# Kernel tuning notes

Measured on AMD Instinct MI355X. Metric: run time of the kernel, lower is better.

Reference implementation:

```python
import jax, jax.numpy as jnp
import numpy as np
import math

N, E, D, H, C, G = 100000, 1600000, 256, 256, 4, 512
LN_EPS = 1e-5


def _pe(n, d):
    # sinusoidal positional encoding, rows = node index
    pos = jnp.arange(n, dtype=jnp.float32)[:, None]                      # [n,1]
    div = jnp.exp(jnp.arange(0, d, 2, dtype=jnp.float32) * (-math.log(10000.0) / d))  # [d/2]
    ang = pos * div                                                      # [n,d/2]
    return jnp.stack([jnp.sin(ang), jnp.cos(ang)], axis=-1).reshape(n, d)


def setup_inputs() -> dict:
    key = jax.random.key(0)
    ks = jax.random.split(key, 24)
    w = lambda k, shp: (jax.random.normal(k, shp, jnp.float32) * 0.05)
    inp = {
        "x": jax.random.normal(ks[0], (N, D), jnp.float32),
        "W_ft": w(ks[1], (D, H)), "b_ft": jnp.zeros((H,), jnp.float32),
        "ln_g": jnp.ones((H,), jnp.float32), "ln_b": jnp.zeros((H,), jnp.float32),
        "W_g0": w(ks[2], (H, H)), "b_g0": jnp.zeros((H,), jnp.float32),
        "W_g1": w(ks[3], (H, H)), "b_g1": jnp.zeros((H,), jnp.float32),
        "W_g2": w(ks[4], (H, H)), "b_g2": jnp.zeros((H,), jnp.float32),
        "W_c0": w(ks[5], (H, H)), "b_c0": jnp.zeros((H,), jnp.float32),
        "W_c1": w(ks[6], (H, H // 2)), "b_c1": jnp.zeros((H // 2,), jnp.float32),
        "W_c2": w(ks[7], (H // 2, C)), "b_c2": jnp.zeros((C,), jnp.float32),
        "edge_index": jax.random.randint(ks[8], (2, E), 0, N, dtype=jnp.int32),
        "batch": jnp.sort(jax.random.randint(ks[9], (N,), 0, G, dtype=jnp.int32)),
    }
    return inp


def reference(x, W_ft, b_ft, ln_g, ln_b, W_g0, b_g0, W_g1, b_g1, W_g2, b_g2,
              W_c0, b_c0, W_c1, b_c1, W_c2, b_c2, edge_index, batch):
    # feature transform: Linear + ReLU + Dropout(eval) + LayerNorm
    h = jax.nn.relu(x @ W_ft + b_ft)
    mu = jnp.mean(h, axis=-1, keepdims=True)
    var = jnp.mean(jnp.square(h - mu), axis=-1, keepdims=True)
    h = (h - mu) * jax.lax.rsqrt(var + LN_EPS) * ln_g + ln_b
    # temporal positional encoding (intended per-node add)
    h = h + _pe(N, H)
    # GCN layers (PyG GCNConv: self-loops + symmetric degree norm + scatter-add)
    loops = jnp.arange(N, dtype=edge_index.dtype)
    src = jnp.concatenate([edge_index[0], loops])
    dst = jnp.concatenate([edge_index[1], loops])
    deg = jax.ops.segment_sum(jnp.ones_like(dst, dtype=h.dtype), dst, num_segments=N)
    dinv = jnp.where(deg > 0, jax.lax.rsqrt(jnp.maximum(deg, 1.0)), 0.0)
    norm = (dinv[src] * dinv[dst])[:, None]                              # [E+N,1]
    for W, b in ((W_g0, b_g0), (W_g1, b_g1), (W_g2, b_g2)):
        m = (h @ W)[src] * norm                                          # gather + scale
        h = jax.nn.relu(jax.ops.segment_sum(m, dst, num_segments=N) + b)
    # global mean pool per graph
    sums = jax.ops.segment_sum(h, batch, num_segments=G)
    cnts = jax.ops.segment_sum(jnp.ones((N,), h.dtype), batch, num_segments=G)
    pooled = sums / jnp.maximum(cnts, 1.0)[:, None]                      # [G,H]
    # classifier MLP
    z = jax.nn.relu(pooled @ W_c0 + b_c0)
    z = jax.nn.relu(z @ W_c1 + b_c1)
    return z @ W_c2 + b_c2                                               # [G,C]
```

## Files before the change

kernel.cpp:

```cpp
#include <hip/hip_runtime.h>
#include <math.h>


typedef __attribute__((ext_vector_type(8))) _Float16 half8;
typedef __attribute__((ext_vector_type(4))) float floatx4;
typedef __attribute__((ext_vector_type(8))) unsigned short us8;

union HU { _Float16 h; unsigned short u; };

static __device__ __forceinline__ unsigned short f2h(float f) {
    HU x; x.h = (_Float16)f; return x.u;
}
static __device__ __forceinline__ float h2f(unsigned short s) {
    HU x; x.u = s; return (float)x.h;
}

static __device__ __forceinline__ void gl_lds16(const void* g, void* l) {
    __builtin_amdgcn_global_load_lds(
        (const __attribute__((address_space(1))) unsigned int*)(g),
        (__attribute__((address_space(3))) unsigned int*)(l), 16, 0, 0);
}

static __device__ __forceinline__ float cw_trig(float ang, bool is_cos) {
    const float i2pi = 0.15915494309189535f;
    const float k = rintf(ang * i2pi);
    float r = fmaf(k, -6.28125f, ang);
    r = fmaf(k, -1.9352436065673828e-3f, r);
    r = fmaf(k, -6.3573019e-8f, r);
    const float rv = r * i2pi;
    return is_cos ? __builtin_amdgcn_cosf(rv) : __builtin_amdgcn_sinf(rv);
}

__global__ void tg_splitB(const float* __restrict__ W0, const float* __restrict__ W1,
                          const float* __restrict__ W2, const float* __restrict__ W3,
                          unsigned short* __restrict__ B0, unsigned short* __restrict__ B1,
                          unsigned short* __restrict__ B2, unsigned short* __restrict__ B3)
{
    const float* Ws[4] = {W0, W1, W2, W3};
    unsigned short* Bs[4] = {B0, B1, B2, B3};
    const float* W = Ws[blockIdx.z];
    unsigned short* Bt = Bs[blockIdx.z];

    __shared__ float T[64][68];
    const int tk = blockIdx.x * 64, tn = blockIdx.y * 64;
    const int t = threadIdx.x;
#pragma unroll
    for (int j = 0; j < 4; ++j) {
        const int idx = t + 256 * j;
        const int k = idx >> 4, c4 = (idx & 15) * 4;
        const float4 v = *(const float4*)&W[(size_t)(tk + k) * 256 + tn + c4];
        T[k][c4] = v.x; T[k][c4 + 1] = v.y; T[k][c4 + 2] = v.z; T[k][c4 + 3] = v.w;
    }
    __syncthreads();
#pragma unroll
    for (int j = 0; j < 4; ++j) {
        const int idx = t + 256 * j;
        const int n = idx >> 4, q = (idx & 15) * 4;
        unsigned short hh[4], ll[4];
#pragma unroll
        for (int i = 0; i < 4; ++i) {
            const float f = T[q + i][n];
            hh[i] = f2h(f);
            ll[i] = f2h(f - h2f(hh[i]));
        }
        uint2 hp, lp;
        hp.x = (unsigned)hh[0] | ((unsigned)hh[1] << 16);
        hp.y = (unsigned)hh[2] | ((unsigned)hh[3] << 16);
        lp.x = (unsigned)ll[0] | ((unsigned)ll[1] << 16);
        lp.y = (unsigned)ll[2] | ((unsigned)ll[3] << 16);
        unsigned short* row = Bt + (size_t)(tn + n) * 512;
        *(uint2*)&row[tk + q]       = hp;
        *(uint2*)&row[256 + tk + q] = lp;
    }
}

__global__ __launch_bounds__(256, 2)
void tg_ft_ln(const float* __restrict__ x, const unsigned short* __restrict__ Bt,
              const float* __restrict__ bias, const float* __restrict__ lng,
              const float* __restrict__ lnb, unsigned short* __restrict__ hh, int N)
{
    __shared__ unsigned short sAh[128 * 64];
    __shared__ unsigned short sAl[128 * 64];
    __shared__ unsigned short sB[256 * 64];
    __shared__ float sStats[128][2][2];
    __shared__ float sDiv[128];

    const int t = threadIdx.x;
    const int w = t >> 6, lane = t & 63;
    const int quad = lane >> 4, l16 = lane & 15;
    const int wr = w >> 1, wc = w & 1;
    const int row0 = blockIdx.x * 128;

    if (t < 128) sDiv[t] = expf((float)(2 * t) * -0.035977892078031970f);

    floatx4 acc[4][8];
#pragma unroll
    for (int i = 0; i < 4; ++i)
#pragma unroll
        for (int j = 0; j < 8; ++j) acc[i][j] = (floatx4){0.f, 0.f, 0.f, 0.f};

    const int arow = t >> 1;
    const int ahalf = t & 1;
    const int srow = lane >> 3;
    const int kgx  = (lane & 7) ^ srow;
    const int rsw  = l16 & 7;

    for (int k4 = 0; k4 < 4; ++k4) {
        const int ka = k4 * 64;
        if (k4) __syncthreads();
#pragma unroll
        for (int i = 0; i < 8; ++i) {
            const int rr = w * 64 + i * 8;
            gl_lds16(Bt + (size_t)(rr + srow) * 512 + ka + kgx * 8, &sB[rr * 64]);
        }
        {
            const int grow = row0 + arow;
            const bool ok = grow < N;
            const float* xp = x + (size_t)grow * 256 + ka + ahalf * 32;
#pragma unroll
            for (int j = 0; j < 4; ++j) {
                const int kg = ahalf * 4 + j;
                float4 v0 = {0.f, 0.f, 0.f, 0.f}, v1 = {0.f, 0.f, 0.f, 0.f};
                if (ok) {
                    v0 = *(const float4*)(xp + j * 8);
                    v1 = *(const float4*)(xp + j * 8 + 4);
                }
                const float f[8] = {v0.x, v0.y, v0.z, v0.w, v1.x, v1.y, v1.z, v1.w};
                us8 hi, lo;
#pragma unroll
                for (int i = 0; i < 8; ++i) {
                    hi[i] = f2h(f[i]);
                    lo[i] = f2h(f[i] - h2f(hi[i]));
                }
                const int ad = arow * 64 + ((kg ^ (arow & 7)) << 3);
                *(us8*)&sAh[ad] = hi;
                *(us8*)&sAl[ad] = lo;
            }
        }
        __syncthreads();
#pragma unroll
        for (int ks = 0; ks < 2; ++ks) {
            const int kq = ks * 4 + quad;
            half8 afh[4], afl[4];
#pragma unroll
            for (int rt = 0; rt < 4; ++rt) {
                const int r = wr * 64 + rt * 16 + l16;
                const int off = r * 64 + ((kq ^ rsw) << 3);
                afh[rt] = *(const half8*)&sAh[off];
                afl[rt] = *(const half8*)&sAl[off];
            }
#pragma unroll
            for (int cb = 0; cb < 2; ++cb) {
                half8 bfr[4];
#pragma unroll
                for (int c4 = 0; c4 < 4; ++c4) {
                    const int n = wc * 128 + (cb * 4 + c4) * 16 + l16;
                    bfr[c4] = *(const half8*)&sB[n * 64 + ((kq ^ rsw) << 3)];
                }
#pragma unroll
                for (int c4 = 0; c4 < 4; ++c4)
#pragma unroll
                    for (int rt = 0; rt < 4; ++rt) {
                        acc[rt][cb * 4 + c4] = __builtin_amdgcn_mfma_f32_16x16x32_f16(
                            afh[rt], bfr[c4], acc[rt][cb * 4 + c4], 0, 0, 0);
                        acc[rt][cb * 4 + c4] = __builtin_amdgcn_mfma_f32_16x16x32_f16(
                            afl[rt], bfr[c4], acc[rt][cb * 4 + c4], 0, 0, 0);
                    }
            }
        }
        __syncthreads();
#pragma unroll
        for (int i = 0; i < 8; ++i) {
            const int rr = w * 64 + i * 8;
            gl_lds16(Bt + (size_t)(rr + srow) * 512 + 256 + ka + kgx * 8, &sB[rr * 64]);
        }
        __syncthreads();
#pragma unroll
        for (int ks = 0; ks < 2; ++ks) {
            const int kq = ks * 4 + quad;
            half8 afh[4];
#pragma unroll
            for (int rt = 0; rt < 4; ++rt) {
                const int r = wr * 64 + rt * 16 + l16;
                afh[rt] = *(const half8*)&sAh[r * 64 + ((kq ^ rsw) << 3)];
            }
#pragma unroll
            for (int cb = 0; cb < 2; ++cb) {
                half8 bfr[4];
#pragma unroll
                for (int c4 = 0; c4 < 4; ++c4) {
                    const int n = wc * 128 + (cb * 4 + c4) * 16 + l16;
                    bfr[c4] = *(const half8*)&sB[n * 64 + ((kq ^ rsw) << 3)];
                }
#pragma unroll
                for (int c4 = 0; c4 < 4; ++c4)
#pragma unroll
                    for (int rt = 0; rt < 4; ++rt)
                        acc[rt][cb * 4 + c4] = __builtin_amdgcn_mfma_f32_16x16x32_f16(
                            afh[rt], bfr[c4], acc[rt][cb * 4 + c4], 0, 0, 0);
            }
        }
    }

    float bs[8], gs[8], bv[8], dv[8];
#pragma unroll
    for (int ct = 0; ct < 8; ++ct) {
        const int gc = wc * 128 + ct * 16 + l16;
        bs[ct] = bias[gc]; gs[ct] = lng[gc]; bv[ct] = lnb[gc];
        dv[ct] = sDiv[gc >> 1];
    }

#pragma unroll
    for (int rt = 0; rt < 4; ++rt) {
#pragma unroll
        for (int i = 0; i < 4; ++i) {
            float s = 0.f, q = 0.f;
#pragma unroll
            for (int ct = 0; ct < 8; ++ct) {
                const float v = fmaxf(acc[rt][ct][i] + bs[ct], 0.f);
                s += v; q += v * v;
            }
#pragma unroll
            for (int m = 1; m < 16; m <<= 1) {
                s += __shfl_xor(s, m, 64);
                q += __shfl_xor(q, m, 64);
            }
            if (l16 == 0) {
                const int rl = wr * 64 + rt * 16 + quad * 4 + i;
                sStats[rl][wc][0] = s;
                sStats[rl][wc][1] = q;
            }
        }
    }
    __syncthreads();

    const bool is_cos = (l16 & 1);
#pragma unroll
    for (int rt = 0; rt < 4; ++rt) {
#pragma unroll
        for (int i = 0; i < 4; ++i) {
            const int rl = wr * 64 + rt * 16 + quad * 4 + i;
            const int gr = row0 + rl;
            if (gr >= N) continue;
            const float sum = sStats[rl][0][0] + sStats[rl][1][0];
            const float sq  = sStats[rl][0][1] + sStats[rl][1][1];
            const float mu  = sum * (1.f / 256.f);
            const float var = sq * (1.f / 256.f) - mu * mu;
            const float rstd = 1.f / sqrtf(var + 1e-5f);
            const float rf = (float)gr;
            unsigned short* orow = hh + (size_t)gr * 256 + wc * 128 + l16;
#pragma unroll
            for (int ct = 0; ct < 8; ++ct) {
                const float v = fmaxf(acc[rt][ct][i] + bs[ct], 0.f);
                const float nrm = (v - mu) * rstd * gs[ct] + bv[ct];
                const float pe = cw_trig(rf * dv[ct], is_cos);
                orow[ct * 16] = f2h(nrm + pe);
            }
        }
    }
}

__global__ __launch_bounds__(256, 3)
void tg_gemm(const unsigned short* __restrict__ Ph,
             const unsigned short* __restrict__ Bt,
             const float* __restrict__ rowscale,
             unsigned short* __restrict__ out)
{
    __shared__ unsigned short sA[128 * 64], sB[128 * 64];

    const int t = threadIdx.x;
    const int w = t >> 6, lane = t & 63;
    const int quad = lane >> 4, l16 = lane & 15;
    const int wr = w >> 1, wc = w & 1;

    const int nwg = gridDim.x;
    const int swq = nwg >> 3, swr = nwg & 7;
    const int xcd = blockIdx.x & 7, oidx = blockIdx.x >> 3;
    const int lg = (xcd < swr ? xcd * (swq + 1)
                              : swr * (swq + 1) + (xcd - swr) * swq) + oidx;
    const int row0 = (lg >> 1) * 128;
    const int col0 = (lg & 1) * 128;

    floatx4 acc[4][4];
#pragma unroll
    for (int i = 0; i < 4; ++i)
#pragma unroll
        for (int j = 0; j < 4; ++j) acc[i][j] = (floatx4){0.f, 0.f, 0.f, 0.f};

    const int srow = lane >> 3;
    const int kgx  = (lane & 7) ^ srow;
    const int rsw  = l16 & 7;

    for (int c = 0; c < 8; ++c) {
        const int ka = (c >> 1) << 6;
        const int kb = ((c & 1) << 8) + ka;
        const bool stA = !(c & 1);
        if (c) __syncthreads();
#pragma unroll
        for (int i = 0; i < 4; ++i) {
            const int rr = w * 32 + i * 8;
            if (stA)
                gl_lds16(Ph + (size_t)(row0 + rr + srow) * 256 + ka + kgx * 8, &sA[rr * 64]);
            gl_lds16(Bt + (size_t)(col0 + rr + srow) * 512 + kb + kgx * 8, &sB[rr * 64]);
        }
        __syncthreads();
#pragma unroll
        for (int ks = 0; ks < 2; ++ks) {
            const int kq = ks * 4 + quad;
            half8 af[4], bfr[4];
#pragma unroll
            for (int rt = 0; rt < 4; ++rt) {
                const int r = wr * 64 + rt * 16 + l16;
                af[rt] = *(const half8*)&sA[r * 64 + ((kq ^ rsw) << 3)];
            }
#pragma unroll
            for (int ct = 0; ct < 4; ++ct) {
                const int n = wc * 64 + ct * 16 + l16;
                bfr[ct] = *(const half8*)&sB[n * 64 + ((kq ^ rsw) << 3)];
            }
#pragma unroll
            for (int ct = 0; ct < 4; ++ct)
#pragma unroll
                for (int rt = 0; rt < 4; ++rt)
                    acc[rt][ct] = __builtin_amdgcn_mfma_f32_16x16x32_f16(
                        af[rt], bfr[ct], acc[rt][ct], 0, 0, 0);
        }
    }

#pragma unroll
    for (int rt = 0; rt < 4; ++rt) {
#pragma unroll
        for (int i = 0; i < 4; ++i) {
            const int gr = row0 + wr * 64 + rt * 16 + quad * 4 + i;
            const float s = rowscale[gr];
#pragma unroll
            for (int ct = 0; ct < 4; ++ct) {
                const int gc = col0 + wc * 64 + ct * 16 + l16;
                out[(size_t)gr * 256 + gc] = f2h(acc[rt][ct][i] * s);
            }
        }
    }
}

__global__ void tg_count(const int* __restrict__ dst, int* __restrict__ deg,
                         int* __restrict__ perm, int E)
{
    const int e = blockIdx.x * blockDim.x + threadIdx.x;
    if (e < E) perm[e] = atomicAdd(&deg[dst[e]], 1);
}

__global__ void tg_dinv(const int* __restrict__ deg, float* __restrict__ dinv, int N)
{
    const int i = blockIdx.x * blockDim.x + threadIdx.x;
    if (i < N) dinv[i] = 1.f / sqrtf((float)(deg[i] + 1));
}

__global__ void tg_scan1(const int* __restrict__ cnt, int* __restrict__ out,
                         int* __restrict__ sums, int N)
{
    __shared__ int tmp[1024];
    const int t = threadIdx.x;
    const int gid = blockIdx.x * 1024 + t;
    const int v = (gid < N) ? cnt[gid] : 0;
    tmp[t] = v;
    __syncthreads();
    for (int o = 1; o < 1024; o <<= 1) {
        const int add = (t >= o) ? tmp[t - o] : 0;
        __syncthreads();
        tmp[t] += add;
        __syncthreads();
    }
    if (gid < N) out[gid] = tmp[t] - v;
    if (t == 1023) sums[blockIdx.x] = tmp[t];
}

__global__ void tg_scan2(int* __restrict__ sums, int nb)
{
    __shared__ int tmp[1024];
    const int t = threadIdx.x;
    const int v = (t < nb) ? sums[t] : 0;
    tmp[t] = v;
    __syncthreads();
    for (int o = 1; o < 1024; o <<= 1) {
        const int add = (t >= o) ? tmp[t - o] : 0;
        __syncthreads();
        tmp[t] += add;
        __syncthreads();
    }
    if (t < nb) sums[t] = tmp[t] - v;
}

__global__ void tg_scan3(int* __restrict__ rowptr, const int* __restrict__ offs,
                         int N, int E)
{
    const int gid = blockIdx.x * 1024 + threadIdx.x;
    if (gid < N) rowptr[gid] += offs[gid >> 10];
    else if (gid == N) rowptr[N] = E;
}

__global__ void tg_fill(const int* __restrict__ src, const int* __restrict__ dst,
                        const int* __restrict__ rowptr, const int* __restrict__ perm,
                        int* __restrict__ col, int E)
{
    const int e = blockIdx.x * blockDim.x + threadIdx.x;
    if (e >= E) return;
    col[rowptr[dst[e]] + perm[e]] = src[e];
}

__global__ void tg_aggregate_h(const unsigned short* __restrict__ hwpb,
                               const int* __restrict__ rowptr, const int* __restrict__ col,
                               const float* __restrict__ dinv, const float* __restrict__ bias,
                               unsigned short* __restrict__ hh, int N)
{
    const int gt = blockIdx.x * blockDim.x + threadIdx.x;
    const int row = gt >> 5;
    if (row >= N) return;
    const int hl = gt & 31;
    const int c = hl * 8;

    const unsigned short* base = hwpb + c;
    const int beg = rowptr[row], end = rowptr[row + 1];

    const us8 sv = *(const us8*)(base + (size_t)row * 256);
    float a[8];
#pragma unroll
    for (int j = 0; j < 8; ++j) a[j] = h2f(sv[j]);

    int p = beg;
    int rem = end - beg;
    int c0[8];
    if (rem >= 8) {
#pragma unroll
        for (int u = 0; u < 8; ++u) c0[u] = col[p + u];
    }
    while (rem >= 8) {
        int c1[8];
        const bool more = rem >= 16;
        if (more) {
#pragma unroll
            for (int u = 0; u < 8; ++u) c1[u] = col[p + 8 + u];
        }
        us8 v[8];
#pragma unroll
        for (int u = 0; u < 8; ++u)
            v[u] = *(const us8*)(base + (size_t)c0[u] * 256);
#pragma unroll
        for (int u = 0; u < 8; ++u)
#pragma unroll
            for (int j = 0; j < 8; ++j) a[j] += h2f(v[u][j]);
        if (more) {
#pragma unroll
            for (int u = 0; u < 8; ++u) c0[u] = c1[u];
        }
        p += 8; rem -= 8;
    }
    if (rem > 0) {
        const int last = end - 1;
        int ci[8];
#pragma unroll
        for (int u = 0; u < 8; ++u) {
            const int pp = (p + u < last) ? p + u : last;
            ci[u] = col[pp];
        }
        us8 v[8];
#pragma unroll
        for (int u = 0; u < 8; ++u)
            v[u] = *(const us8*)(base + (size_t)(u < rem ? ci[u] : row) * 256);
#pragma unroll
        for (int u = 0; u < 8; ++u) {
            if (u < rem) {
#pragma unroll
                for (int j = 0; j < 8; ++j) a[j] += h2f(v[u][j]);
            }
        }
    }

    const float di = dinv[row];
    const float4 b0 = *(const float4*)&bias[c];
    const float4 b1 = *(const float4*)&bias[c + 4];
    us8 o;
    o[0] = f2h(fmaxf(di * a[0] + b0.x, 0.f));
    o[1] = f2h(fmaxf(di * a[1] + b0.y, 0.f));
    o[2] = f2h(fmaxf(di * a[2] + b0.z, 0.f));
    o[3] = f2h(fmaxf(di * a[3] + b0.w, 0.f));
    o[4] = f2h(fmaxf(di * a[4] + b1.x, 0.f));
    o[5] = f2h(fmaxf(di * a[5] + b1.y, 0.f));
    o[6] = f2h(fmaxf(di * a[6] + b1.z, 0.f));
    o[7] = f2h(fmaxf(di * a[7] + b1.w, 0.f));
    *(us8*)&hh[(size_t)row * 256 + c] = o;
}

__global__ void tg_ranges(const int* __restrict__ batch, int* __restrict__ starts,
                          int N, int G)
{
    const int g = blockIdx.x * blockDim.x + threadIdx.x;
    if (g > G) return;
    int lo = 0, hi = N;
    while (lo < hi) {
        const int mid = (lo + hi) >> 1;
        if (batch[mid] < g) lo = mid + 1; else hi = mid;
    }
    starts[g] = lo;
}

__global__ void tg_pool(const unsigned short* __restrict__ hh,
                        const int* __restrict__ starts, float* __restrict__ pooled, int G)
{
    __shared__ float sh[4][64][4];
    const int g = blockIdx.x;
    const int t = threadIdx.x;
    const int wv = t >> 6, lane = t & 63;
    const int c = lane * 4;
    const int beg = starts[g], end = starts[g + 1];
    float s0 = 0.f, s1 = 0.f, s2 = 0.f, s3 = 0.f;
    for (int r = beg + wv; r < end; r += 4) {
        const ushort4 vh = *(const ushort4*)&hh[(size_t)r * 256 + c];
        s0 += h2f(vh.x); s1 += h2f(vh.y); s2 += h2f(vh.z); s3 += h2f(vh.w);
    }
    sh[wv][lane][0] = s0; sh[wv][lane][1] = s1;
    sh[wv][lane][2] = s2; sh[wv][lane][3] = s3;
    __syncthreads();
    if (t < 64) {
        const float inv = 1.f / fmaxf((float)(end - beg), 1.f);
        float4 o;
        o.x = (sh[0][t][0] + sh[1][t][0] + sh[2][t][0] + sh[3][t][0]) * inv;
        o.y = (sh[0][t][1] + sh[1][t][1] + sh[2][t][1] + sh[3][t][1]) * inv;
        o.z = (sh[0][t][2] + sh[1][t][2] + sh[2][t][2] + sh[3][t][2]) * inv;
        o.w = (sh[0][t][3] + sh[1][t][3] + sh[2][t][3] + sh[3][t][3]) * inv;
        *(float4*)&pooled[(size_t)g * 256 + t * 4] = o;
    }
}

__global__ void tg_mlp(const float* __restrict__ A, const float* __restrict__ B,
                       const float* __restrict__ bias, float* __restrict__ Cout,
                       int M, int K, int Nc, int do_relu)
{
    const int idx = blockIdx.x * blockDim.x + threadIdx.x;
    if (idx >= M * Nc) return;
    const int m = idx / Nc;
    const int n = idx - m * Nc;
    float acc = 0.f;
    for (int k = 0; k < K; ++k) acc += A[(size_t)m * K + k] * B[(size_t)k * Nc + n];
    acc += bias[n];
    Cout[idx] = do_relu ? fmaxf(acc, 0.f) : acc;
}

extern "C" void kernel_launch(void* const* d_in, const int* in_sizes, int n_in,
                              void* d_out, int out_size, void* d_ws, size_t ws_size,
                              hipStream_t stream)
{
    const float* x    = (const float*)d_in[0];
    const float* W_ft = (const float*)d_in[1];
    const float* b_ft = (const float*)d_in[2];
    const float* ln_g = (const float*)d_in[3];
    const float* ln_b = (const float*)d_in[4];
    const float* W_g[3] = {(const float*)d_in[5], (const float*)d_in[7], (const float*)d_in[9]};
    const float* b_g[3] = {(const float*)d_in[6], (const float*)d_in[8], (const float*)d_in[10]};
    const float* W_c0 = (const float*)d_in[11];
    const float* b_c0 = (const float*)d_in[12];
    const float* W_c1 = (const float*)d_in[13];
    const float* b_c1 = (const float*)d_in[14];
    const float* W_c2 = (const float*)d_in[15];
    const float* b_c2 = (const float*)d_in[16];
    const int*   edge  = (const int*)d_in[17];
    const int*   batch = (const int*)d_in[18];

    const int N    = in_sizes[18];
    const int E    = in_sizes[17] / 2;
    const int Mpad = (N + 127) & ~127;
    const int H2   = in_sizes[14];
    const int Cc   = in_sizes[15] / H2;
    const int G    = out_size / Cc;

    const int* srcI = edge;
    const int* dstI = edge + E;

    size_t off = 0;
    auto alloc = [&](size_t bytes) {
        char* p = (char*)d_ws + off;
        off = (off + bytes + 255) & ~(size_t)255;
        return p;
    };
    unsigned short* hh   = (unsigned short*)alloc((size_t)Mpad * 256 * 2);
    unsigned short* hwpb = (unsigned short*)alloc((size_t)Mpad * 256 * 2);
    float* dinv   = (float*)alloc((size_t)Mpad * 4);
    int*   deg    = (int*)alloc((size_t)Mpad * 4);
    int*   rowptr = (int*)alloc((size_t)(N + 1) * 4);
    int*   perm   = (int*)alloc((size_t)E * 4);
    int*   col    = (int*)alloc((size_t)E * 4);
    int*   bsums  = (int*)alloc(1024 * 4);
    int*   starts = (int*)alloc((size_t)(G + 1) * 4);
    float* pooled = (float*)alloc((size_t)G * 256 * 4);
    float* z0     = (float*)alloc((size_t)G * 256 * 4);
    float* z1     = (float*)alloc((size_t)G * H2 * 4);
    unsigned short* Bt[4];
    for (int i = 0; i < 4; ++i)
        Bt[i] = (unsigned short*)alloc((size_t)256 * 512 * 2);
    (void)ws_size; (void)n_in;

    hipMemsetAsync(deg, 0, (size_t)Mpad * 4, stream);
    hipMemsetAsync(hh + (size_t)N * 256, 0, (size_t)(Mpad - N) * 256 * 2, stream);

    tg_splitB<<<dim3(4, 4, 4), dim3(256), 0, stream>>>(
        W_ft, W_g[0], W_g[1], W_g[2], Bt[0], Bt[1], Bt[2], Bt[3]);

    tg_ft_ln<<<dim3(Mpad / 128), dim3(256), 0, stream>>>(
        x, Bt[0], b_ft, ln_g, ln_b, hh, N);

    tg_count<<<dim3((E + 255) / 256), dim3(256), 0, stream>>>(dstI, deg, perm, E);
    tg_dinv<<<dim3((Mpad + 255) / 256), dim3(256), 0, stream>>>(deg, dinv, Mpad);
    const int NB = (N + 1023) / 1024;
    tg_scan1<<<dim3(NB), dim3(1024), 0, stream>>>(deg, rowptr, bsums, N);
    tg_scan2<<<dim3(1), dim3(1024), 0, stream>>>(bsums, NB);
    tg_scan3<<<dim3((N + 1024) / 1024), dim3(1024), 0, stream>>>(rowptr, bsums, N, E);
    tg_fill<<<dim3((E + 255) / 256), dim3(256), 0, stream>>>(srcI, dstI, rowptr, perm, col, E);

    const int nbx = (Mpad / 128) * 2;
    for (int l = 0; l < 3; ++l) {
        tg_gemm<<<dim3(nbx), dim3(256), 0, stream>>>(hh, Bt[l + 1], dinv, hwpb);
        tg_aggregate_h<<<dim3((N + 7) / 8), dim3(256), 0, stream>>>(hwpb, rowptr, col, dinv,
                                                                    b_g[l], hh, N);
    }

    tg_ranges<<<dim3((G + 256) / 256), dim3(256), 0, stream>>>(batch, starts, N, G);
    tg_pool<<<dim3(G), dim3(256), 0, stream>>>(hh, starts, pooled, G);

    tg_mlp<<<dim3((G * 256 + 255) / 256), dim3(256), 0, stream>>>(pooled, W_c0, b_c0, z0, G, 256, 256, 1);
    tg_mlp<<<dim3((G * H2 + 255) / 256), dim3(256), 0, stream>>>(z0, W_c1, b_c1, z1, G, 256, H2, 1);
    tg_mlp<<<dim3((G * Cc + 255) / 256), dim3(256), 0, stream>>>(z1, W_c2, b_c2, (float*)d_out, G, H2, Cc, 0);
}
```

Baseline: 1.061 ms.

## Fuse GCN aggregation with next-layer GEMM and merge pooling/MLP kernels

```diff
diff --git a/kernel.cpp b/kernel.cpp
--- a/kernel.cpp
+++ b/kernel.cpp
@@ -337,6 +337,167 @@
             for (int ct = 0; ct < 4; ++ct) {
                 const int gc = col0 + wc * 64 + ct * 16 + l16;
                 out[(size_t)gr * 256 + gc] = f2h(acc[rt][ct][i] * s);
+            }
+        }
+    }
+}
+
+__global__ __launch_bounds__(512, 4)
+void tg_agg_gemm(const unsigned short* __restrict__ hwpIn,
+                 const int* __restrict__ rowptr, const int* __restrict__ col,
+                 const float* __restrict__ dinv, const float* __restrict__ bias,
+                 const unsigned short* __restrict__ Bt,
+                 unsigned short* __restrict__ hwpOut, int N)
+{
+    __shared__ unsigned short hA[128 * 256];
+    __shared__ unsigned short sB[128 * 64];
+
+    const int t = threadIdx.x;
+    const int row0 = blockIdx.x * 128;
+
+    {
+        const int g = t >> 5;
+        const int hl = t & 31;
+        const int c = hl * 8;
+        const unsigned short* base = hwpIn + c;
+        for (int it = 0; it < 8; ++it) {
+            const int lr = g * 8 + it;
+            const int row = row0 + lr;
+            us8 o = {0, 0, 0, 0, 0, 0, 0, 0};
+            if (row < N) {
+                const int beg = rowptr[row], end = rowptr[row + 1];
+                const us8 sv = *(const us8*)(base + (size_t)row * 256);
+                float a[8];
+#pragma unroll
+                for (int j = 0; j < 8; ++j) a[j] = h2f(sv[j]);
+                int p = beg;
+                int rem = end - beg;
+                int c0[8];
+                if (rem >= 8) {
+#pragma unroll
+                    for (int u = 0; u < 8; ++u) c0[u] = col[p + u];
+                }
+                while (rem >= 8) {
+                    int c1[8];
+                    const bool more = rem >= 16;
+                    if (more) {
+#pragma unroll
+                        for (int u = 0; u < 8; ++u) c1[u] = col[p + 8 + u];
+                    }
+                    us8 v[8];
+#pragma unroll
+                    for (int u = 0; u < 8; ++u)
+                        v[u] = *(const us8*)(base + (size_t)c0[u] * 256);
+#pragma unroll
+                    for (int u = 0; u < 8; ++u)
+#pragma unroll
+                        for (int j = 0; j < 8; ++j) a[j] += h2f(v[u][j]);
+                    if (more) {
+#pragma unroll
+                        for (int u = 0; u < 8; ++u) c0[u] = c1[u];
+                    }
+                    p += 8; rem -= 8;
+                }
+                if (rem > 0) {
+                    const int last = end - 1;
+                    int ci[8];
+#pragma unroll
+                    for (int u = 0; u < 8; ++u) {
+                        const int pp = (p + u < last) ? p + u : last;
+                        ci[u] = col[pp];
+                    }
+                    us8 v[8];
+#pragma unroll
+                    for (int u = 0; u < 8; ++u)
+                        v[u] = *(const us8*)(base + (size_t)(u < rem ? ci[u] : row) * 256);
+#pragma unroll
+                    for (int u = 0; u < 8; ++u) {
+                        if (u < rem) {
+#pragma unroll
+                            for (int j = 0; j < 8; ++j) a[j] += h2f(v[u][j]);
+                        }
+                    }
+                }
+                const float di = dinv[row];
+                const float4 b0 = *(const float4*)&bias[c];
+                const float4 b1 = *(const float4*)&bias[c + 4];
+                o[0] = f2h(fmaxf(di * a[0] + b0.x, 0.f));
+                o[1] = f2h(fmaxf(di * a[1] + b0.y, 0.f));
+                o[2] = f2h(fmaxf(di * a[2] + b0.z, 0.f));
+                o[3] = f2h(fmaxf(di * a[3] + b0.w, 0.f));
+                o[4] = f2h(fmaxf(di * a[4] + b1.x, 0.f));
+                o[5] = f2h(fmaxf(di * a[5] + b1.y, 0.f));
+                o[6] = f2h(fmaxf(di * a[6] + b1.z, 0.f));
+                o[7] = f2h(fmaxf(di * a[7] + b1.w, 0.f));
+            }
+            const int ad = lr * 256 + (c & ~63) + (((hl & 7) ^ (lr & 7)) << 3);
+            *(us8*)&hA[ad] = o;
+        }
+    }
+    __syncthreads();
+
+    const int w = t >> 6, lane = t & 63;
+    const int quad = lane >> 4, l16 = lane & 15;
+    const int rb = (w & 1) * 64;
+    const int cq = (w >> 1) * 32;
+    const int srow = lane >> 3;
+    const int kgx  = (lane & 7) ^ srow;
+    const int rsw  = l16 & 7;
+
+    floatx4 acc[4][4];
+#pragma unroll
+    for (int i = 0; i < 4; ++i)
+#pragma unroll
+        for (int j = 0; j < 4; ++j) acc[i][j] = (floatx4){0.f, 0.f, 0.f, 0.f};
+
+    for (int c8 = 0; c8 < 8; ++c8) {
+        const int ka = (c8 >> 1) << 6;
+        const int kb = ((c8 & 1) << 8) + ka;
+#pragma unroll
+        for (int h = 0; h < 2; ++h) {
+            if (c8 || h) __syncthreads();
+            {
+                const int rr = w * 16;
+                gl_lds16(Bt + (size_t)(h * 128 + rr + srow) * 512 + kb + kgx * 8,
+                         &sB[rr * 64]);
+                gl_lds16(Bt + (size_t)(h * 128 + rr + 8 + srow) * 512 + kb + kgx * 8,
+                         &sB[(rr + 8) * 64]);
+            }
+            __syncthreads();
+#pragma unroll
+            for (int ks = 0; ks < 2; ++ks) {
+                const int kq = ks * 4 + quad;
+                half8 af[4], bf[2];
+#pragma unroll
+                for (int rt = 0; rt < 4; ++rt) {
+                    const int r = rb + rt * 16 + l16;
+                    af[rt] = *(const half8*)&hA[r * 256 + ka + ((kq ^ rsw) << 3)];
+                }
+#pragma unroll
+                for (int ct = 0; ct < 2; ++ct) {
+                    const int br = cq + ct * 16 + l16;
+                    bf[ct] = *(const half8*)&sB[br * 64 + ((kq ^ rsw) << 3)];
+                }
+#pragma unroll
+                for (int ct = 0; ct < 2; ++ct)
+#pragma unroll
+                    for (int rt = 0; rt < 4; ++rt)
+                        acc[rt][h * 2 + ct] = __builtin_amdgcn_mfma_f32_16x16x32_f16(
+                            af[rt], bf[ct], acc[rt][h * 2 + ct], 0, 0, 0);
+            }
+        }
+    }
+
+#pragma unroll
+    for (int rt = 0; rt < 4; ++rt) {
+#pragma unroll
+        for (int i = 0; i < 4; ++i) {
+            const int gr = row0 + rb + rt * 16 + quad * 4 + i;
+            const float s = dinv[gr];
+#pragma unroll
+            for (int j = 0; j < 4; ++j) {
+                const int gc = (j >> 1) * 128 + cq + (j & 1) * 16 + l16;
+                hwpOut[(size_t)gr * 256 + gc] = f2h(acc[rt][j][i] * s);
             }
         }
     }
@@ -490,28 +651,27 @@
     *(us8*)&hh[(size_t)row * 256 + c] = o;
 }
 
-__global__ void tg_ranges(const int* __restrict__ batch, int* __restrict__ starts,
-                          int N, int G)
-{
-    const int g = blockIdx.x * blockDim.x + threadIdx.x;
-    if (g > G) return;
-    int lo = 0, hi = N;
-    while (lo < hi) {
-        const int mid = (lo + hi) >> 1;
-        if (batch[mid] < g) lo = mid + 1; else hi = mid;
-    }
-    starts[g] = lo;
-}
-
 __global__ void tg_pool(const unsigned short* __restrict__ hh,
-                        const int* __restrict__ starts, float* __restrict__ pooled, int G)
+                        const int* __restrict__ batch, float* __restrict__ pooled,
+                        int N, int G)
 {
     __shared__ float sh[4][64][4];
+    __shared__ int sBE[2];
     const int g = blockIdx.x;
     const int t = threadIdx.x;
+    if (t < 2) {
+        const int target = g + t;
+        int lo = 0, hi = N;
+        while (lo < hi) {
+            const int mid = (lo + hi) >> 1;
+            if (batch[mid] < target) lo = mid + 1; else hi = mid;
+        }
+        sBE[t] = lo;
+    }
+    __syncthreads();
+    const int beg = sBE[0], end = sBE[1];
     const int wv = t >> 6, lane = t & 63;
     const int c = lane * 4;
-    const int beg = starts[g], end = starts[g + 1];
     float s0 = 0.f, s1 = 0.f, s2 = 0.f, s3 = 0.f;
     for (int r = beg + wv; r < end; r += 4) {
         const ushort4 vh = *(const ushort4*)&hh[(size_t)r * 256 + c];
@@ -531,18 +691,35 @@
     }
 }
 
-__global__ void tg_mlp(const float* __restrict__ A, const float* __restrict__ B,
-                       const float* __restrict__ bias, float* __restrict__ Cout,
-                       int M, int K, int Nc, int do_relu)
-{
-    const int idx = blockIdx.x * blockDim.x + threadIdx.x;
-    if (idx >= M * Nc) return;
-    const int m = idx / Nc;
-    const int n = idx - m * Nc;
-    float acc = 0.f;
-    for (int k = 0; k < K; ++k) acc += A[(size_t)m * K + k] * B[(size_t)k * Nc + n];
-    acc += bias[n];
-    Cout[idx] = do_relu ? fmaxf(acc, 0.f) : acc;
+__global__ __launch_bounds__(256)
+void tg_mlp3(const float* __restrict__ pooled,
+             const float* __restrict__ W0, const float* __restrict__ b0,
+             const float* __restrict__ W1, const float* __restrict__ b1,
+             const float* __restrict__ W2, const float* __restrict__ b2,
+             float* __restrict__ out, int H2, int Cc)
+{
+    __shared__ float zin[256];
+    __shared__ float z0[256];
+    __shared__ float z1[256];
+    const int g = blockIdx.x;
+    const int t = threadIdx.x;
+    zin[t] = pooled[(size_t)g * 256 + t];
+    __syncthreads();
+    float a = 0.f;
+    for (int k = 0; k < 256; ++k) a += zin[k] * W0[(size_t)k * 256 + t];
+    z0[t] = fmaxf(a + b0[t], 0.f);
+    __syncthreads();
+    if (t < H2) {
+        float a1 = 0.f;
+        for (int k = 0; k < 256; ++k) a1 += z0[k] * W1[(size_t)k * H2 + t];
+        z1[t] = fmaxf(a1 + b1[t], 0.f);
+    }
+    __syncthreads();
+    if (t < Cc) {
+        float a2 = 0.f;
+        for (int k = 0; k < H2; ++k) a2 += z1[k] * W2[(size_t)k * Cc + t];
+        out[(size_t)g * Cc + t] = a2 + b2[t];
+    }
 }
 
 extern "C" void kernel_launch(void* const* d_in, const int* in_sizes, int n_in,
@@ -581,18 +758,16 @@
         off = (off + bytes + 255) & ~(size_t)255;
         return p;
     };
-    unsigned short* hh   = (unsigned short*)alloc((size_t)Mpad * 256 * 2);
-    unsigned short* hwpb = (unsigned short*)alloc((size_t)Mpad * 256 * 2);
+    unsigned short* hh    = (unsigned short*)alloc((size_t)Mpad * 256 * 2);
+    unsigned short* hwpbA = (unsigned short*)alloc((size_t)Mpad * 256 * 2);
+    unsigned short* hwpbB = (unsigned short*)alloc((size_t)Mpad * 256 * 2);
     float* dinv   = (float*)alloc((size_t)Mpad * 4);
     int*   deg    = (int*)alloc((size_t)Mpad * 4);
     int*   rowptr = (int*)alloc((size_t)(N + 1) * 4);
     int*   perm   = (int*)alloc((size_t)E * 4);
     int*   col    = (int*)alloc((size_t)E * 4);
     int*   bsums  = (int*)alloc(1024 * 4);
-    int*   starts = (int*)alloc((size_t)(G + 1) * 4);
     float* pooled = (float*)alloc((size_t)G * 256 * 4);
-    float* z0     = (float*)alloc((size_t)G * 256 * 4);
-    float* z1     = (float*)alloc((size_t)G * H2 * 4);
     unsigned short* Bt[4];
     for (int i = 0; i < 4; ++i)
         Bt[i] = (unsigned short*)alloc((size_t)256 * 512 * 2);
@@ -616,16 +791,17 @@
     tg_fill<<<dim3((E + 255) / 256), dim3(256), 0, stream>>>(srcI, dstI, rowptr, perm, col, E);
 
     const int nbx = (Mpad / 128) * 2;
-    for (int l = 0; l < 3; ++l) {
-        tg_gemm<<<dim3(nbx), dim3(256), 0, stream>>>(hh, Bt[l + 1], dinv, hwpb);
-        tg_aggregate_h<<<dim3((N + 7) / 8), dim3(256), 0, stream>>>(hwpb, rowptr, col, dinv,
-                                                                    b_g[l], hh, N);
-    }
-
-    tg_ranges<<<dim3((G + 256) / 256), dim3(256), 0, stream>>>(batch, starts, N, G);
-    tg_pool<<<dim3(G), dim3(256), 0, stream>>>(hh, starts, pooled, G);
-
-    tg_mlp<<<dim3((G * 256 + 255) / 256), dim3(256), 0, stream>>>(pooled, W_c0, b_c0, z0, G, 256, 256, 1);
-    tg_mlp<<<dim3((G * H2 + 255) / 256), dim3(256), 0, stream>>>(z0, W_c1, b_c1, z1, G, 256, H2, 1);
-    tg_mlp<<<dim3((G * Cc + 255) / 256), dim3(256), 0, stream>>>(z1, W_c2, b_c2, (float*)d_out, G, H2, Cc, 0);
-}
+    tg_gemm<<<dim3(nbx), dim3(256), 0, stream>>>(hh, Bt[1], dinv, hwpbA);
+    const int nfb = Mpad / 128;
+    tg_agg_gemm<<<dim3(nfb), dim3(512), 0, stream>>>(hwpbA, rowptr, col, dinv,
+                                                     b_g[0], Bt[2], hwpbB, N);
+    tg_agg_gemm<<<dim3(nfb), dim3(512), 0, stream>>>(hwpbB, rowptr, col, dinv,
+                                                     b_g[1], Bt[3], hwpbA, N);
+    tg_aggregate_h<<<dim3((N + 7) / 8), dim3(256), 0, stream>>>(hwpbA, rowptr, col, dinv,
+                                                                b_g[2], hh, N);
+
+    tg_pool<<<dim3(G), dim3(256), 0, stream>>>(hh, batch, pooled, N, G);
+
+    tg_mlp3<<<dim3(G), dim3(256), 0, stream>>>(pooled, W_c0, b_c0, W_c1, b_c1,
+                                               W_c2, b_c2, (float*)d_out, H2, Cc);
+}
```

Result: faster. 924.1 us (-12.9%).

## Slice aggregation by column groups and split CSR neighbors by source half

Applied to the files above, without the earlier changes.

```diff
diff --git a/kernel.cpp b/kernel.cpp
--- a/kernel.cpp
+++ b/kernel.cpp
@@ -342,142 +342,59 @@
     }
 }
 
-__global__ void tg_count(const int* __restrict__ dst, int* __restrict__ deg,
-                         int* __restrict__ perm, int E)
-{
-    const int e = blockIdx.x * blockDim.x + threadIdx.x;
-    if (e < E) perm[e] = atomicAdd(&deg[dst[e]], 1);
-}
-
-__global__ void tg_dinv(const int* __restrict__ deg, float* __restrict__ dinv, int N)
-{
-    const int i = blockIdx.x * blockDim.x + threadIdx.x;
-    if (i < N) dinv[i] = 1.f / sqrtf((float)(deg[i] + 1));
-}
-
-__global__ void tg_scan1(const int* __restrict__ cnt, int* __restrict__ out,
-                         int* __restrict__ sums, int N)
-{
-    __shared__ int tmp[1024];
-    const int t = threadIdx.x;
-    const int gid = blockIdx.x * 1024 + t;
-    const int v = (gid < N) ? cnt[gid] : 0;
-    tmp[t] = v;
-    __syncthreads();
-    for (int o = 1; o < 1024; o <<= 1) {
-        const int add = (t >= o) ? tmp[t - o] : 0;
-        __syncthreads();
-        tmp[t] += add;
-        __syncthreads();
-    }
-    if (gid < N) out[gid] = tmp[t] - v;
-    if (t == 1023) sums[blockIdx.x] = tmp[t];
-}
-
-__global__ void tg_scan2(int* __restrict__ sums, int nb)
-{
-    __shared__ int tmp[1024];
-    const int t = threadIdx.x;
-    const int v = (t < nb) ? sums[t] : 0;
-    tmp[t] = v;
-    __syncthreads();
-    for (int o = 1; o < 1024; o <<= 1) {
-        const int add = (t >= o) ? tmp[t - o] : 0;
-        __syncthreads();
-        tmp[t] += add;
-        __syncthreads();
-    }
-    if (t < nb) sums[t] = tmp[t] - v;
-}
-
-__global__ void tg_scan3(int* __restrict__ rowptr, const int* __restrict__ offs,
-                         int N, int E)
-{
-    const int gid = blockIdx.x * 1024 + threadIdx.x;
-    if (gid < N) rowptr[gid] += offs[gid >> 10];
-    else if (gid == N) rowptr[N] = E;
-}
-
-__global__ void tg_fill(const int* __restrict__ src, const int* __restrict__ dst,
-                        const int* __restrict__ rowptr, const int* __restrict__ perm,
-                        int* __restrict__ col, int E)
-{
-    const int e = blockIdx.x * blockDim.x + threadIdx.x;
-    if (e >= E) return;
-    col[rowptr[dst[e]] + perm[e]] = src[e];
-}
-
-__global__ void tg_aggregate_h(const unsigned short* __restrict__ hwpb,
-                               const int* __restrict__ rowptr, const int* __restrict__ col,
-                               const float* __restrict__ dinv, const float* __restrict__ bias,
-                               unsigned short* __restrict__ hh, int N)
-{
-    const int gt = blockIdx.x * blockDim.x + threadIdx.x;
-    const int row = gt >> 5;
+__global__ __launch_bounds__(256, 4)
+void tg_agg_sliced(const unsigned short* __restrict__ hwpIn,
+                   const int* __restrict__ rowptr, const int* __restrict__ degLow,
+                   const int* __restrict__ col, const float* __restrict__ dinv,
+                   const float* __restrict__ bias,
+                   unsigned short* __restrict__ out, int N)
+{
+    const int slice = blockIdx.x & 7;
+    const int rt    = blockIdx.x >> 3;
+    const int t = threadIdx.x;
+    const int w = t >> 6, lane = t & 63;
+    const int row = rt * 64 + w * 16 + (lane >> 2);
     if (row >= N) return;
-    const int hl = gt & 31;
-    const int c = hl * 8;
-
-    const unsigned short* base = hwpb + c;
-    const int beg = rowptr[row], end = rowptr[row + 1];
+    const int q = lane & 3;
+    const int cb = slice * 32 + q * 8;
+
+    const unsigned short* base = hwpIn + cb;
 
     const us8 sv = *(const us8*)(base + (size_t)row * 256);
     float a[8];
 #pragma unroll
     for (int j = 0; j < 8; ++j) a[j] = h2f(sv[j]);
 
-    int p = beg;
-    int rem = end - beg;
-    int c0[8];
-    if (rem >= 8) {
-#pragma unroll
-        for (int u = 0; u < 8; ++u) c0[u] = col[p + u];
-    }
-    while (rem >= 8) {
-        int c1[8];
-        const bool more = rem >= 16;
-        if (more) {
-#pragma unroll
-            for (int u = 0; u < 8; ++u) c1[u] = col[p + 8 + u];
-        }
-        us8 v[8];
-#pragma unroll
-        for (int u = 0; u < 8; ++u)
-            v[u] = *(const us8*)(base + (size_t)c0[u] * 256);
-#pragma unroll
-        for (int u = 0; u < 8; ++u)
-#pragma unroll
-            for (int j = 0; j < 8; ++j) a[j] += h2f(v[u][j]);
-        if (more) {
-#pragma unroll
-            for (int u = 0; u < 8; ++u) c0[u] = c1[u];
-        }
-        p += 8; rem -= 8;
-    }
-    if (rem > 0) {
-        const int last = end - 1;
-        int ci[8];
-#pragma unroll
-        for (int u = 0; u < 8; ++u) {
-            const int pp = (p + u < last) ? p + u : last;
-            ci[u] = col[pp];
-        }
-        us8 v[8];
-#pragma unroll
-        for (int u = 0; u < 8; ++u)
-            v[u] = *(const us8*)(base + (size_t)(u < rem ? ci[u] : row) * 256);
-#pragma unroll
-        for (int u = 0; u < 8; ++u) {
-            if (u < rem) {
-#pragma unroll
-                for (int j = 0; j < 8; ++j) a[j] += h2f(v[u][j]);
-            }
-        }
-    }
+    const int beg = rowptr[row];
+    const int end = rowptr[row + 1];
+    const int mid = beg + degLow[row];
+
+    auto do_seg = [&](int p0, int pe) {
+        for (int p = p0; p < pe; p += 4) {
+            const int nn = pe - p;
+            int cid[4];
+#pragma unroll
+            for (int u = 0; u < 4; ++u)
+                if (u < nn) cid[u] = col[p + u];
+            us8 vv[4];
+#pragma unroll
+            for (int u = 0; u < 4; ++u)
+                if (u < nn) vv[u] = *(const us8*)(base + (size_t)cid[u] * 256);
+#pragma unroll
+            for (int u = 0; u < 4; ++u) {
+                if (u < nn) {
+#pragma unroll
+                    for (int j = 0; j < 8; ++j) a[j] += h2f(vv[u][j]);
+                }
+            }
+        }
+    };
+    do_seg(beg, mid);
+    do_seg(mid, end);
 
     const float di = dinv[row];
-    const float4 b0 = *(const float4*)&bias[c];
-    const float4 b1 = *(const float4*)&bias[c + 4];
+    const float4 b0 = *(const float4*)&bias[cb];
+    const float4 b1 = *(const float4*)&bias[cb + 4];
     us8 o;
     o[0] = f2h(fmaxf(di * a[0] + b0.x, 0.f));
     o[1] = f2h(fmaxf(di * a[1] + b0.y, 0.f));
@@ -487,31 +404,104 @@
     o[5] = f2h(fmaxf(di * a[5] + b1.y, 0.f));
     o[6] = f2h(fmaxf(di * a[6] + b1.z, 0.f));
     o[7] = f2h(fmaxf(di * a[7] + b1.w, 0.f));
-    *(us8*)&hh[(size_t)row * 256 + c] = o;
-}
-
-__global__ void tg_ranges(const int* __restrict__ batch, int* __restrict__ starts,
-                          int N, int G)
-{
-    const int g = blockIdx.x * blockDim.x + threadIdx.x;
-    if (g > G) return;
-    int lo = 0, hi = N;
-    while (lo < hi) {
-        const int mid = (lo + hi) >> 1;
-        if (batch[mid] < g) lo = mid + 1; else hi = mid;
-    }
-    starts[g] = lo;
+    *(us8*)&out[(size_t)row * 256 + cb] = o;
+}
+
+__global__ void tg_count(const int* __restrict__ src, const int* __restrict__ dst,
+                         int* __restrict__ degLow, int* __restrict__ degHigh,
+                         int* __restrict__ perm, int E, int half)
+{
+    const int e = blockIdx.x * blockDim.x + threadIdx.x;
+    if (e >= E) return;
+    const int d = dst[e];
+    if (src[e] < half) perm[e] = atomicAdd(&degLow[d], 1);
+    else               perm[e] = atomicAdd(&degHigh[d], 1);
+}
+
+__global__ void tg_dinv(const int* __restrict__ degLow, const int* __restrict__ degHigh,
+                        float* __restrict__ dinv, int N)
+{
+    const int i = blockIdx.x * blockDim.x + threadIdx.x;
+    if (i < N) dinv[i] = 1.f / sqrtf((float)(degLow[i] + degHigh[i] + 1));
+}
+
+__global__ void tg_scan1(const int* __restrict__ cntA, const int* __restrict__ cntB,
+                         int* __restrict__ out, int* __restrict__ sums, int N)
+{
+    __shared__ int tmp[1024];
+    const int t = threadIdx.x;
+    const int gid = blockIdx.x * 1024 + t;
+    const int v = (gid < N) ? (cntA[gid] + cntB[gid]) : 0;
+    tmp[t] = v;
+    __syncthreads();
+    for (int o = 1; o < 1024; o <<= 1) {
+        const int add = (t >= o) ? tmp[t - o] : 0;
+        __syncthreads();
+        tmp[t] += add;
+        __syncthreads();
+    }
+    if (gid < N) out[gid] = tmp[t] - v;
+    if (t == 1023) sums[blockIdx.x] = tmp[t];
+}
+
+__global__ void tg_scan2(int* __restrict__ sums, int nb)
+{
+    __shared__ int tmp[1024];
+    const int t = threadIdx.x;
+    const int v = (t < nb) ? sums[t] : 0;
+    tmp[t] = v;
+    __syncthreads();
+    for (int o = 1; o < 1024; o <<= 1) {
+        const int add = (t >= o) ? tmp[t - o] : 0;
+        __syncthreads();
+        tmp[t] += add;
+        __syncthreads();
+    }
+    if (t < nb) sums[t] = tmp[t] - v;
+}
+
+__global__ void tg_scan3(int* __restrict__ rowptr, const int* __restrict__ offs,
+                         int N, int E)
+{
+    const int gid = blockIdx.x * 1024 + threadIdx.x;
+    if (gid < N) rowptr[gid] += offs[gid >> 10];
+    else if (gid == N) rowptr[N] = E;
+}
+
+__global__ void tg_fill(const int* __restrict__ src, const int* __restrict__ dst,
+                        const int* __restrict__ rowptr, const int* __restrict__ degLow,
+                        const int* __restrict__ perm, int* __restrict__ col,
+                        int E, int half)
+{
+    const int e = blockIdx.x * blockDim.x + threadIdx.x;
+    if (e >= E) return;
+    const int s = src[e];
+    const int d = dst[e];
+    const int pos = (s < half) ? perm[e] : degLow[d] + perm[e];
+    col[rowptr[d] + pos] = s;
 }
 
 __global__ void tg_pool(const unsigned short* __restrict__ hh,
-                        const int* __restrict__ starts, float* __restrict__ pooled, int G)
+                        const int* __restrict__ batch, float* __restrict__ pooled,
+                        int N, int G)
 {
     __shared__ float sh[4][64][4];
+    __shared__ int sBE[2];
     const int g = blockIdx.x;
     const int t = threadIdx.x;
+    if (t < 2) {
+        const int target = g + t;
+        int lo = 0, hi = N;
+        while (lo < hi) {
+            const int mid = (lo + hi) >> 1;
+            if (batch[mid] < target) lo = mid + 1; else hi = mid;
+        }
+        sBE[t] = lo;
+    }
+    __syncthreads();
+    const int beg = sBE[0], end = sBE[1];
     const int wv = t >> 6, lane = t & 63;
     const int c = lane * 4;
-    const int beg = starts[g], end = starts[g + 1];
     float s0 = 0.f, s1 = 0.f, s2 = 0.f, s3 = 0.f;
     for (int r = beg + wv; r < end; r += 4) {
         const ushort4 vh = *(const ushort4*)&hh[(size_t)r * 256 + c];
@@ -531,18 +521,35 @@
     }
 }
 
-__global__ void tg_mlp(const float* __restrict__ A, const float* __restrict__ B,
-                       const float* __restrict__ bias, float* __restrict__ Cout,
-                       int M, int K, int Nc, int do_relu)
-{
-    const int idx = blockIdx.x * blockDim.x + threadIdx.x;
-    if (idx >= M * Nc) return;
-    const int m = idx / Nc;
-    const int n = idx - m * Nc;
-    float acc = 0.f;
-    for (int k = 0; k < K; ++k) acc += A[(size_t)m * K + k] * B[(size_t)k * Nc + n];
-    acc += bias[n];
-    Cout[idx] = do_relu ? fmaxf(acc, 0.f) : acc;
+__global__ __launch_bounds__(256)
+void tg_mlp3(const float* __restrict__ pooled,
+             const float* __restrict__ W0, const float* __restrict__ b0,
+             const float* __restrict__ W1, const float* __restrict__ b1,
+             const float* __restrict__ W2, const float* __restrict__ b2,
+             float* __restrict__ out, int H2, int Cc)
+{
+    __shared__ float zin[256];
+    __shared__ float z0[256];
+    __shared__ float z1[256];
+    const int g = blockIdx.x;
+    const int t = threadIdx.x;
+    zin[t] = pooled[(size_t)g * 256 + t];
+    __syncthreads();
+    float a = 0.f;
+    for (int k = 0; k < 256; ++k) a += zin[k] * W0[(size_t)k * 256 + t];
+    z0[t] = fmaxf(a + b0[t], 0.f);
+    __syncthreads();
+    if (t < H2) {
+        float a1 = 0.f;
+        for (int k = 0; k < 256; ++k) a1 += z0[k] * W1[(size_t)k * H2 + t];
+        z1[t] = fmaxf(a1 + b1[t], 0.f);
+    }
+    __syncthreads();
+    if (t < Cc) {
+        float a2 = 0.f;
+        for (int k = 0; k < H2; ++k) a2 += z1[k] * W2[(size_t)k * Cc + t];
+        out[(size_t)g * Cc + t] = a2 + b2[t];
+    }
 }
 
 extern "C" void kernel_launch(void* const* d_in, const int* in_sizes, int n_in,
@@ -571,6 +578,7 @@
     const int H2   = in_sizes[14];
     const int Cc   = in_sizes[15] / H2;
     const int G    = out_size / Cc;
+    const int half = N >> 1;
 
     const int* srcI = edge;
     const int* dstI = edge + E;
@@ -581,25 +589,26 @@
         off = (off + bytes + 255) & ~(size_t)255;
         return p;
     };
-    unsigned short* hh   = (unsigned short*)alloc((size_t)Mpad * 256 * 2);
-    unsigned short* hwpb = (unsigned short*)alloc((size_t)Mpad * 256 * 2);
-    float* dinv   = (float*)alloc((size_t)Mpad * 4);
-    int*   deg    = (int*)alloc((size_t)Mpad * 4);
-    int*   rowptr = (int*)alloc((size_t)(N + 1) * 4);
-    int*   perm   = (int*)alloc((size_t)E * 4);
-    int*   col    = (int*)alloc((size_t)E * 4);
-    int*   bsums  = (int*)alloc(1024 * 4);
-    int*   starts = (int*)alloc((size_t)(G + 1) * 4);
-    float* pooled = (float*)alloc((size_t)G * 256 * 4);
-    float* z0     = (float*)alloc((size_t)G * 256 * 4);
-    float* z1     = (float*)alloc((size_t)G * H2 * 4);
+    unsigned short* hh  = (unsigned short*)alloc((size_t)Mpad * 256 * 2);
+    unsigned short* P   = (unsigned short*)alloc((size_t)Mpad * 256 * 2);
+    unsigned short* Q   = (unsigned short*)alloc((size_t)Mpad * 256 * 2);
+    float* dinv    = (float*)alloc((size_t)Mpad * 4);
+    int*   degLow  = (int*)alloc((size_t)Mpad * 4);
+    int*   degHigh = (int*)alloc((size_t)Mpad * 4);
+    int*   rowptr  = (int*)alloc((size_t)(N + 1) * 4);
+    int*   perm    = (int*)alloc((size_t)E * 4);
+    int*   col     = (int*)alloc((size_t)E * 4);
+    int*   bsums   = (int*)alloc(1024 * 4);
+    float* pooled  = (float*)alloc((size_t)G * 256 * 4);
     unsigned short* Bt[4];
     for (int i = 0; i < 4; ++i)
         Bt[i] = (unsigned short*)alloc((size_t)256 * 512 * 2);
     (void)ws_size; (void)n_in;
 
-    hipMemsetAsync(deg, 0, (size_t)Mpad * 4, stream);
+    hipMemsetAsync(degLow, 0, (size_t)Mpad * 4, stream);
+    hipMemsetAsync(degHigh, 0, (size_t)Mpad * 4, stream);
     hipMemsetAsync(hh + (size_t)N * 256, 0, (size_t)(Mpad - N) * 256 * 2, stream);
+    hipMemsetAsync(Q + (size_t)N * 256, 0, (size_t)(Mpad - N) * 256 * 2, stream);
 
     tg_splitB<<<dim3(4, 4, 4), dim3(256), 0, stream>>>(
         W_ft, W_g[0], W_g[1], W_g[2], Bt[0], Bt[1], Bt[2], Bt[3]);
@@ -607,25 +616,30 @@
     tg_ft_ln<<<dim3(Mpad / 128), dim3(256), 0, stream>>>(
         x, Bt[0], b_ft, ln_g, ln_b, hh, N);
 
-    tg_count<<<dim3((E + 255) / 256), dim3(256), 0, stream>>>(dstI, deg, perm, E);
-    tg_dinv<<<dim3((Mpad + 255) / 256), dim3(256), 0, stream>>>(deg, dinv, Mpad);
+    tg_count<<<dim3((E + 255) / 256), dim3(256), 0, stream>>>(
+        srcI, dstI, degLow, degHigh, perm, E, half);
+    tg_dinv<<<dim3((Mpad + 255) / 256), dim3(256), 0, stream>>>(degLow, degHigh, dinv, Mpad);
     const int NB = (N + 1023) / 1024;
-    tg_scan1<<<dim3(NB), dim3(1024), 0, stream>>>(deg, rowptr, bsums, N);
+    tg_scan1<<<dim3(NB), dim3(1024), 0, stream>>>(degLow, degHigh, rowptr, bsums, N);
     tg_scan2<<<dim3(1), dim3(1024), 0, stream>>>(bsums, NB);
     tg_scan3<<<dim3((N + 1024) / 1024), dim3(1024), 0, stream>>>(rowptr, bsums, N, E);
-    tg_fill<<<dim3((E + 255) / 256), dim3(256), 0, stream>>>(srcI, dstI, rowptr, perm, col, E);
+    tg_fill<<<dim3((E + 255) / 256), dim3(256), 0, stream>>>(
+        srcI, dstI, rowptr, degLow, perm, col, E, half);
 
     const int nbx = (Mpad / 128) * 2;
-    for (int l = 0; l < 3; ++l) {
-        tg_gemm<<<dim3(nbx), dim3(256), 0, stream>>>(hh, Bt[l + 1], dinv, hwpb);
-        tg_aggregate_h<<<dim3((N + 7) / 8), dim3(256), 0, stream>>>(hwpb, rowptr, col, dinv,
-                                                                    b_g[l], hh, N);
-    }
-
-    tg_ranges<<<dim3((G + 256) / 256), dim3(256), 0, stream>>>(batch, starts, N, G);
-    tg_pool<<<dim3(G), dim3(256), 0, stream>>>(hh, starts, pooled, G);
-
-    tg_mlp<<<dim3((G * 256 + 255) / 256), dim3(256), 0, stream>>>(pooled, W_c0, b_c0, z0, G, 256, 256, 1);
-    tg_mlp<<<dim3((G * H2 + 255) / 256), dim3(256), 0, stream>>>(z0, W_c1, b_c1, z1, G, 256, H2, 1);
-    tg_mlp<<<dim3((G * Cc + 255) / 256), dim3(256), 0, stream>>>(z1, W_c2, b_c2, (float*)d_out, G, H2, Cc, 0);
-}
+    const int nag = (Mpad / 64) * 8;
+    tg_gemm<<<dim3(nbx), dim3(256), 0, stream>>>(hh, Bt[1], dinv, P);
+    tg_agg_sliced<<<dim3(nag), dim3(256), 0, stream>>>(P, rowptr, degLow, col,
+                                                       dinv, b_g[0], Q, N);
+    tg_gemm<<<dim3(nbx), dim3(256), 0, stream>>>(Q, Bt[2], dinv, P);
+    tg_agg_sliced<<<dim3(nag), dim3(256), 0, stream>>>(P, rowptr, degLow, col,
+                                                       dinv, b_g[1], Q, N);
+    tg_gemm<<<dim3(nbx), dim3(256), 0, stream>>>(Q, Bt[3], dinv, P);
+    tg_agg_sliced<<<dim3(nag), dim3(256), 0, stream>>>(P, rowptr, degLow, col,
+                                                       dinv, b_g[2], hh, N);
+
+    tg_pool<<<dim3(G), dim3(256), 0, stream>>>(hh, batch, pooled, N, G);
+
+    tg_mlp3<<<dim3(G), dim3(256), 0, stream>>>(pooled, W_c0, b_c0, W_c1, b_c1,
+                                               W_c2, b_c2, (float*)d_out, H2, Cc);
+}
```

New measurement: 1.116 ms. 5.1% more time.
